# Performance work log

Measured on AMD Instinct MI355X. Metric: run time of the kernel, lower is better.

## Reference

```python
import jax, jax.numpy as jnp
import numpy as np

NOISE_DIM = 64
SEQ_DIM = 64
HIDDEN = 512
BATCH = 1024
N_STEPS = 512
INPUT_SIZE = SEQ_DIM + NOISE_DIM + 1  # 129


def setup_inputs() -> dict:
    key = jax.random.key(0)
    ks = jax.random.split(key, 8)
    s = 0.05
    return {
        "noise": jax.random.normal(ks[0], (BATCH, N_STEPS, NOISE_DIM), dtype=jnp.float32),
        "dts": jax.random.uniform(ks[1], (BATCH, N_STEPS, 1), dtype=jnp.float32),
        "W_ih": jax.random.normal(ks[2], (4 * HIDDEN, INPUT_SIZE), dtype=jnp.float32) * s,
        "W_hh": jax.random.normal(ks[3], (4 * HIDDEN, HIDDEN), dtype=jnp.float32) * s,
        "b_ih": jax.random.normal(ks[4], (4 * HIDDEN,), dtype=jnp.float32) * s,
        "b_hh": jax.random.normal(ks[5], (4 * HIDDEN,), dtype=jnp.float32) * s,
        "W_out": jax.random.normal(ks[6], (SEQ_DIM, HIDDEN), dtype=jnp.float32) * s,
        "b_out": jax.random.normal(ks[7], (SEQ_DIM,), dtype=jnp.float32) * s,
    }


def reference(noise, dts, W_ih, W_hh, b_ih, b_hh, W_out, b_out):
    B = noise.shape[0]
    H = W_hh.shape[1]
    last0 = jnp.zeros((B, SEQ_DIM), dtype=noise.dtype)
    h0 = jnp.zeros((B, H), dtype=noise.dtype)
    c0 = jnp.zeros((B, H), dtype=noise.dtype)
    b = b_ih + b_hh

    def step(carry, inp):
        last, h, c = carry
        n_t, dt_t = inp  # (B, noise_dim), (B, 1)
        x = jnp.concatenate([last, n_t, dt_t], axis=-1)  # (B, input_size)
        gates = x @ W_ih.T + h @ W_hh.T + b  # (B, 4H)
        i_g, f_g, g_g, o_g = jnp.split(gates, 4, axis=-1)
        c_new = jax.nn.sigmoid(f_g) * c + jax.nn.sigmoid(i_g) * jnp.tanh(g_g)
        h_new = jax.nn.sigmoid(o_g) * jnp.tanh(c_new)
        y = h_new @ W_out.T + b_out  # (B, seq_dim)
        return (y, h_new, c_new), y

    noise_t = jnp.swapaxes(noise, 0, 1)  # (n, B, noise_dim)
    dts_t = jnp.swapaxes(dts, 0, 1)  # (n, B, 1)
    (last, h, c), ys = jax.lax.scan(step, (last0, h0, c0), (noise_t, dts_t))
    gen_seq = jnp.swapaxes(ys, 0, 1)  # (B, n, seq_dim)
    return gen_seq, h[None, :, :], c[None, :, :]
```

## Files before the change

kernel.cpp:

```cpp
#include <hip/hip_runtime.h>
#include <stdint.h>


#define NGRP 32
#define KF_X 5
#define KF_H 32
#define KF_TOT 37
#define MAIN_FRAGS (8 * 8 * KF_TOT)
#define Y_FRAGS 64
#define TOT_FRAGS (MAIN_FRAGS + Y_FRAGS)
#define HOFF 33554432ull
#define COFF (HOFF + 524288ull)

typedef __attribute__((ext_vector_type(8))) short short8;
typedef __attribute__((ext_vector_type(4))) float f32x4;
typedef __attribute__((ext_vector_type(16))) float f32x16;
typedef __attribute__((ext_vector_type(4))) unsigned int u32x4;

__device__ __forceinline__ unsigned short f2bf(float x) {
  unsigned int u = __float_as_uint(x);
  u += 0x7FFFu + ((u >> 16) & 1u);
  return (unsigned short)(u >> 16);
}
__device__ __forceinline__ unsigned int pk2(float a, float b) {
  return (unsigned)f2bf(a) | ((unsigned)f2bf(b) << 16);
}
__device__ __forceinline__ int uperm(int kz, int hi, int j) {
  return 64 * (kz >> 2) + 16 * (kz & 3) + 8 * (j >> 2) + 2 * (j & 3) + hi;
}

__global__ void prep_pack(const float* __restrict__ Wih,
                          const float* __restrict__ Whh,
                          const float* __restrict__ bih,
                          const float* __restrict__ bhh,
                          const float* __restrict__ Wout,
                          const float* __restrict__ bout,
                          unsigned short* __restrict__ pack,
                          int* __restrict__ flags) {
  int tid = blockIdx.x * blockDim.x + threadIdx.x;
  if (blockIdx.x == 0) {
    for (int i = threadIdx.x; i < NGRP * 256; i += blockDim.x) flags[i] = 0;
  }
  int fi = tid >> 6, l = tid & 63;
  if (fi >= TOT_FRAGS) return;
  int r = l & 31, hi = l >> 5;
  unsigned short o[8];
  if (fi < MAIN_FRAGS) {
    int jwg = fi / (8 * KF_TOT);
    int rem = fi % (8 * KF_TOT);
    int w = rem / KF_TOT, kf = rem % KF_TOT;
    int g2 = r & 3, s = r >> 3, hb = (r >> 2) & 1;
    int row = g2 * 512 + jwg * 64 + w * 8 + 2 * s + hb;
    for (int j = 0; j < 8; ++j) {
      float v;
      if (kf < KF_X) {
        int kx = kf * 16 + 8 * hi + j;
        if (kx < 64) {
          v = Wih[row * 129 + 64 + kx];
        } else if (kx == 64) {
          v = Wih[row * 129 + 128];
        } else if (kx == 65) {
          float a = bih[row] + bhh[row];
          for (int q = 0; q < 64; ++q) a += Wih[row * 129 + q] * bout[q];
          v = a;
        } else if (kx == 66) {
          float a = 0.f;
          for (int q = 0; q < 64; ++q) a -= Wih[row * 129 + q] * bout[q];
          v = a;
        } else {
          v = 0.f;
        }
      } else {
        int kz = kf - KF_X;
        int U = uperm(kz, hi, j);
        float a = Whh[row * 512 + U];
        for (int q = 0; q < 64; ++q) a += Wih[row * 129 + q] * Wout[q * 512 + U];
        v = a;
      }
      o[j] = f2bf(v);
    }
  } else {
    int fy = fi - MAIN_FRAGS;
    int ry = fy >> 5, kz = fy & 31;
    int row = ry * 32 + r;
    for (int j = 0; j < 8; ++j) {
      int U = uperm(kz, hi, j);
      o[j] = f2bf(Wout[row * 512 + U]);
    }
  }
  unsigned short* dst = pack + (size_t)fi * 512 + l * 8;
  for (int j = 0; j < 8; ++j) dst[j] = o[j];
}

#define AGLD(p) \
  __hip_atomic_load((p), __ATOMIC_RELAXED, __HIP_MEMORY_SCOPE_AGENT)
#define AGST(p, v) \
  __hip_atomic_store((p), (v), __ATOMIC_RELAXED, __HIP_MEMORY_SCOPE_AGENT)

__global__ __launch_bounds__(256)
__attribute__((amdgpu_waves_per_eu(1, 1))) void lstm_main(
    const float* __restrict__ noise, const float* __restrict__ dts,
    const unsigned short* __restrict__ pack, const float* __restrict__ bout,
    unsigned short* __restrict__ hbuf, int* __restrict__ flags,
    float* __restrict__ out) {
  __shared__ __align__(16) unsigned short act[KF_TOT * 512];
  __shared__ __align__(16) float ybuf[4 * 64 * 17];
  const int tid = threadIdx.x;
  const int w = tid >> 6, l = tid & 63;
  const int r = l & 31, hi = l >> 5;
  const int bid = blockIdx.x;
  const int jwg = bid >> 5, grp = bid & 31;
  const int bat = grp * 32 + r;

  for (int i = tid; i < (KF_H * 512) / 2; i += 256)
    ((unsigned int*)(act + KF_X * 512))[i] = 0u;

  short8 wA[KF_TOT], wB[KF_TOT];
  {
    const unsigned short* wl =
        pack + (size_t)((jwg * 8 + 2 * w) * KF_TOT) * 512 + l * 8;
#pragma unroll
    for (int kf = 0; kf < KF_TOT; ++kf) {
      wA[kf] = *(const short8*)(wl + (size_t)kf * 512);
      asm volatile("" : "+a"(wA[kf]));
      wB[kf] = *(const short8*)(wl + (size_t)(KF_TOT + kf) * 512);
      if (kf < 16)
        asm volatile("" : "+a"(wB[kf]));
      else
        asm volatile("" : "+v"(wB[kf]));
    }
  }

  float c0[4] = {0.f, 0.f, 0.f, 0.f}, c1[4] = {0.f, 0.f, 0.f, 0.f};
  float h0[4] = {0.f, 0.f, 0.f, 0.f}, h1[4] = {0.f, 0.f, 0.f, 0.f};
  float4 bo = {0.f, 0.f, 0.f, 0.f};
  if (jwg < 2) bo = *(const float4*)(bout + 32 * jwg + 8 * w + 4 * hi);

  auto cell = [&](const f32x16& a, float* cs, float* hs) {
#pragma unroll
    for (int s = 0; s < 4; ++s) {
      float iv = a[4 * s + 0], fv = a[4 * s + 1];
      float gv = a[4 * s + 2], ov = a[4 * s + 3];
      float ig = 1.f / (1.f + __expf(-iv));
      float fg = 1.f / (1.f + __expf(-fv));
      float e2g = __expf(2.f * gv);
      float gg = 1.f - 2.f / (e2g + 1.f);
      float og = 1.f / (1.f + __expf(-ov));
      float cn = fg * cs[s] + ig * gg;
      float e2c = __expf(2.f * cn);
      float tc = 1.f - 2.f / (e2c + 1.f);
      cs[s] = cn;
      hs[s] = og * tc;
    }
  };

  auto y_partial = [&]() {
    const unsigned short* yl =
        pack + (size_t)(MAIN_FRAGS + jwg * 32 + w * 8) * 512 + l * 8;
    f32x16 ya;
#pragma unroll
    for (int i = 0; i < 16; ++i) ya[i] = 0.f;
    short8 ywr[4];
#pragma unroll
    for (int p = 0; p < 4; ++p) ywr[p] = *(const short8*)(yl + (size_t)p * 512);
#pragma unroll
    for (int q = 0; q < 8; ++q) {
      short8 bv = *(const short8*)&act[(KF_X + w * 8 + q) * 512 + l * 8];
      ya = __builtin_amdgcn_mfma_f32_32x32x16_bf16(ywr[q & 3], bv, ya, 0, 0, 0);
      if (q + 4 < 8)
        ywr[q & 3] = *(const short8*)(yl + (size_t)(q + 4) * 512);
    }
#pragma unroll
    for (int s = 0; s < 4; ++s) {
      f32x4 v = {ya[4 * s], ya[4 * s + 1], ya[4 * s + 2], ya[4 * s + 3]};
      *(f32x4*)&ybuf[(w * 64 + l) * 17 + 4 * s] = v;
    }
  };

  auto y_sum = [&](int tw) {
    f32x4 s0 = *(f32x4*)&ybuf[(0 * 64 + l) * 17 + 4 * w];
    f32x4 s1 = *(f32x4*)&ybuf[(1 * 64 + l) * 17 + 4 * w];
    f32x4 s2 = *(f32x4*)&ybuf[(2 * 64 + l) * 17 + 4 * w];
    f32x4 s3 = *(f32x4*)&ybuf[(3 * 64 + l) * 17 + 4 * w];
    float4 o;
    o.x = s0[0] + s1[0] + s2[0] + s3[0] + bo.x;
    o.y = s0[1] + s1[1] + s2[1] + s3[1] + bo.y;
    o.z = s0[2] + s1[2] + s2[2] + s3[2] + bo.z;
    o.w = s0[3] + s1[3] + s2[3] + s3[3] + bo.w;
    *(float4*)(out + ((size_t)bat * 512 + tw) * 64 + 32 * jwg + 8 * w +
               4 * hi) = o;
  };

  {
    const float* np = noise + (size_t)bat * 512 * 64 + w * 16 + 8 * hi;
    float4 f0 = *(const float4*)np;
    float4 f1 = *(const float4*)(np + 4);
    u32x4 d;
    d[0] = pk2(f0.x, f0.y);
    d[1] = pk2(f0.z, f0.w);
    d[2] = pk2(f1.x, f1.y);
    d[3] = pk2(f1.z, f1.w);
    *(u32x4*)&act[w * 512 + l * 8] = d;
    if (w == 0) {
      u32x4 d4 = {0u, 0u, 0u, 0u};
      if (hi == 0) {
        float dt = dts[(size_t)bat * 512];
        d4[0] = pk2(dt, 1.0f);
        d4[1] = pk2(1.0f, 0.0f);
      }
      *(u32x4*)&act[4 * 512 + l * 8] = d4;
    }
  }
  __syncthreads();

  const int kz_own = 4 * jwg + w;

#pragma unroll 1
  for (int t = 0; t < 512; ++t) {
    float4 nf0, nf1;
    float dtv = 0.f;
    if (t < 511) {
      const float* np =
          noise + ((size_t)bat * 512 + t + 1) * 64 + w * 16 + 8 * hi;
      nf0 = *(const float4*)np;
      nf1 = *(const float4*)(np + 4);
      if (w == 0 && hi == 0) dtv = dts[(size_t)bat * 512 + t + 1];
    }

    f32x16 a0, a1;
#pragma unroll
    for (int i = 0; i < 16; ++i) {
      a0[i] = 0.f;
      a1[i] = 0.f;
    }
#pragma unroll
    for (int kf = 0; kf < KF_TOT; ++kf) {
      short8 bv = *(const short8*)&act[kf * 512 + l * 8];
      a0 = __builtin_amdgcn_mfma_f32_32x32x16_bf16(wA[kf], bv, a0, 0, 0, 0);
      a1 = __builtin_amdgcn_mfma_f32_32x32x16_bf16(wB[kf], bv, a1, 0, 0, 0);
    }

    cell(a0, c0, h0);
    cell(a1, c1, h1);

    unsigned int p0 = pk2(h0[0], h0[1]), p1 = pk2(h0[2], h0[3]);
    unsigned int p2 = pk2(h1[0], h1[1]), p3 = pk2(h1[2], h1[3]);
    {
      unsigned long long* hp = (unsigned long long*)(
          hbuf + ((size_t)(grp * 2 + (t & 1)) * KF_H + kz_own) * 512 + l * 8);
      AGST(hp, (unsigned long long)p0 | ((unsigned long long)p1 << 32));
      AGST(hp + 1, (unsigned long long)p2 | ((unsigned long long)p3 << 32));
    }

    if (jwg < 2 && t > 0) y_partial();

    __syncthreads();

    if (tid == 0) AGST(&flags[grp * 256 + jwg * 32], t + 1);

    if (jwg < 2 && t > 0) y_sum(t - 1);

    if (t < 511) {
      u32x4 d;
      d[0] = pk2(nf0.x, nf0.y);
      d[1] = pk2(nf0.z, nf0.w);
      d[2] = pk2(nf1.x, nf1.y);
      d[3] = pk2(nf1.z, nf1.w);
      *(u32x4*)&act[w * 512 + l * 8] = d;
      if (w == 0) {
        u32x4 d4 = {0u, 0u, 0u, 0u};
        if (hi == 0) d4[0] = pk2(dtv, 1.0f);
        *(u32x4*)&act[4 * 512 + l * 8] = d4;
      }
    }

    if (tid < 8) {
      while (AGLD(&flags[grp * 256 + tid * 32]) < t + 1)
        __builtin_amdgcn_s_sleep(1);
    }
    __syncthreads();

    {
      const unsigned long long* src = (const unsigned long long*)(
          hbuf + (size_t)(grp * 2 + (t & 1)) * KF_H * 512);
      unsigned long long q[16];
#pragma unroll
      for (int k = 0; k < 8; ++k) {
        int idx = (4 * k + w) * 128 + l * 2;
        q[2 * k] = AGLD(src + idx);
        q[2 * k + 1] = AGLD(src + idx + 1);
      }
#pragma unroll
      for (int k = 0; k < 8; ++k) {
        u32x4 d;
        d[0] = (unsigned)q[2 * k];
        d[1] = (unsigned)(q[2 * k] >> 32);
        d[2] = (unsigned)q[2 * k + 1];
        d[3] = (unsigned)(q[2 * k + 1] >> 32);
        *(u32x4*)&act[(KF_X + 4 * k + w) * 512 + l * 8] = d;
      }
    }
    __syncthreads();
  }

  if (jwg < 2) y_partial();
  __syncthreads();
  if (jwg < 2) y_sum(511);
#pragma unroll
  for (int s = 0; s < 4; ++s) {
    int U0 = jwg * 64 + (2 * w + 0) * 8 + 2 * s + hi;
    int U1 = jwg * 64 + (2 * w + 1) * 8 + 2 * s + hi;
    out[HOFF + (size_t)bat * 512 + U0] = h0[s];
    out[COFF + (size_t)bat * 512 + U0] = c0[s];
    out[HOFF + (size_t)bat * 512 + U1] = h1[s];
    out[COFF + (size_t)bat * 512 + U1] = c1[s];
  }
}

extern "C" void kernel_launch(void* const* d_in, const int* in_sizes, int n_in,
                              void* d_out, int out_size, void* d_ws,
                              size_t ws_size, hipStream_t stream) {
  (void)in_sizes;
  (void)n_in;
  (void)out_size;
  (void)ws_size;
  const float* noise = (const float*)d_in[0];
  const float* dts = (const float*)d_in[1];
  const float* Wih = (const float*)d_in[2];
  const float* Whh = (const float*)d_in[3];
  const float* bih = (const float*)d_in[4];
  const float* bhh = (const float*)d_in[5];
  const float* Wout = (const float*)d_in[6];
  const float* bout = (const float*)d_in[7];

  unsigned short* pack = (unsigned short*)d_ws;
  unsigned short* hbuf = pack + (size_t)TOT_FRAGS * 512;
  int* flags = (int*)(hbuf + (size_t)NGRP * 2 * KF_H * 512);

  prep_pack<<<(TOT_FRAGS * 64 + 255) / 256, 256, 0, stream>>>(
      Wih, Whh, bih, bhh, Wout, bout, pack, flags);
  lstm_main<<<256, 256, 0, stream>>>(noise, dts, pack, bout, hbuf, flags,
                                     (float*)d_out);
}
```

Baseline: 2.788 ms.

## Add XCC-local fast path for inter-block hidden-state exchange with fallback

Each block records its XCC id. When all 8 blocks of a batch group share one XCC and the workspace is large enough, they exchange hidden state and step flags through a second buffer using sc0-scoped stores and loads, which should stay in that XCC's L2 instead of going through agent-scope coherence. Every step also keeps writing the agent-scope buffer and flags. If the agent-scope flag shows up before the fast one, a trip flag switches the block back to the slow path. This adds duplicate stores, a full vmcnt wait before each barrier, and fragile assumptions about cache coherence.

```diff
diff --git a/kernel.cpp b/kernel.cpp
--- a/kernel.cpp
+++ b/kernel.cpp
@@ -36,10 +36,13 @@
                           const float* __restrict__ Wout,
                           const float* __restrict__ bout,
                           unsigned short* __restrict__ pack,
-                          int* __restrict__ flags) {
+                          int* __restrict__ flags, int* __restrict__ flags2) {
   int tid = blockIdx.x * blockDim.x + threadIdx.x;
   if (blockIdx.x == 0) {
-    for (int i = threadIdx.x; i < NGRP * 256; i += blockDim.x) flags[i] = 0;
+    for (int i = threadIdx.x; i < NGRP * 256; i += blockDim.x) {
+      flags[i] = 0;
+      flags2[i] = 0;
+    }
   }
   int fi = tid >> 6, l = tid & 63;
   if (fi >= TOT_FRAGS) return;
@@ -101,16 +104,26 @@
 __attribute__((amdgpu_waves_per_eu(1, 1))) void lstm_main(
     const float* __restrict__ noise, const float* __restrict__ dts,
     const unsigned short* __restrict__ pack, const float* __restrict__ bout,
-    unsigned short* __restrict__ hbuf, int* __restrict__ flags,
+    unsigned short* __restrict__ hbuf, unsigned short* __restrict__ hbuf2,
+    int* __restrict__ flags, int* __restrict__ flags2, int fastEnable,
     float* __restrict__ out) {
   __shared__ __align__(16) unsigned short act[KF_TOT * 512];
   __shared__ __align__(16) float ybuf[4 * 64 * 17];
+  __shared__ int xshare[8];
+  __shared__ int tripflag;
   const int tid = threadIdx.x;
   const int w = tid >> 6, l = tid & 63;
   const int r = l & 31, hi = l >> 5;
   const int bid = blockIdx.x;
   const int jwg = bid >> 5, grp = bid & 31;
   const int bat = grp * 32 + r;
+  const int fbase = grp * 256;
+
+  if (tid == 0) {
+    unsigned xcc = __builtin_amdgcn_s_getreg((31u << 11) | 20u) & 0xFFu;
+    AGST(&flags2[fbase + jwg * 32 + 16], (int)xcc + 1);
+    tripflag = 0;
+  }
 
   for (int i = tid; i < (KF_H * 512) / 2; i += 256)
     ((unsigned int*)(act + KF_X * 512))[i] = 0u;
@@ -214,9 +227,13 @@
   __syncthreads();
 
   const int kz_own = 4 * jwg + w;
+  bool fast_ok = false;
+  int verdictNew = 0;
 
 #pragma unroll 1
   for (int t = 0; t < 512; ++t) {
+    const int par = t & 1;
+
     float4 nf0, nf1;
     float dtv = 0.f;
     if (t < 511) {
@@ -247,16 +264,37 @@
     unsigned int p2 = pk2(h1[0], h1[1]), p3 = pk2(h1[2], h1[3]);
     {
       unsigned long long* hp = (unsigned long long*)(
-          hbuf + ((size_t)(grp * 2 + (t & 1)) * KF_H + kz_own) * 512 + l * 8);
+          hbuf2 + ((size_t)(grp * 2 + par) * KF_H + kz_own) * 512 + l * 8);
       AGST(hp, (unsigned long long)p0 | ((unsigned long long)p1 << 32));
       AGST(hp + 1, (unsigned long long)p2 | ((unsigned long long)p3 << 32));
+      if (fast_ok) {
+        u32x4 pay;
+        pay[0] = p0;
+        pay[1] = p1;
+        pay[2] = p2;
+        pay[3] = p3;
+        unsigned long long wa =
+            (unsigned long long)hbuf + (unsigned long long)(grp * 2 + par) * 32768ull +
+            (unsigned long long)kz_own * 1024ull + (unsigned long long)l * 16ull;
+        asm volatile("global_store_dwordx4 %0, %1, off sc0" ::"v"(wa), "v"(pay)
+                     : "memory");
+      }
     }
 
     if (jwg < 2 && t > 0) y_partial();
 
+    asm volatile("s_waitcnt vmcnt(0)" ::: "memory");
     __syncthreads();
 
-    if (tid == 0) AGST(&flags[grp * 256 + jwg * 32], t + 1);
+    if (tid == 0) {
+      AGST(&flags2[fbase + jwg * 32], t + 1);
+      if (fast_ok) {
+        unsigned long long fa = (unsigned long long)&flags[fbase + jwg * 32];
+        unsigned tg = (unsigned)(t + 1);
+        asm volatile("global_store_dword %0, %1, off sc0" ::"v"(fa), "v"(tg)
+                     : "memory");
+      }
+    }
 
     if (jwg < 2 && t > 0) y_sum(t - 1);
 
@@ -274,15 +312,77 @@
       }
     }
 
-    if (tid < 8) {
-      while (AGLD(&flags[grp * 256 + tid * 32]) < t + 1)
-        __builtin_amdgcn_s_sleep(1);
+    if (fast_ok) {
+      if (tid < 8) {
+        unsigned long long fa = (unsigned long long)&flags[fbase + tid * 32];
+        const int* f2p = &flags2[fbase + tid * 32];
+        while (1) {
+          unsigned v;
+          asm volatile(
+              "global_load_dword %0, %1, off sc0\n\ts_waitcnt vmcnt(0)"
+              : "=v"(v)
+              : "v"(fa)
+              : "memory");
+          if ((int)v >= t + 1) break;
+          if (AGLD(f2p) >= t + 1) {
+            tripflag = 1;
+            break;
+          }
+        }
+      }
+    } else {
+      if (tid < 8) {
+        while (AGLD(&flags2[fbase + tid * 32]) < t + 1)
+          __builtin_amdgcn_s_sleep(1);
+        if (t == 0) xshare[tid] = AGLD(&flags2[fbase + tid * 32 + 16]);
+      }
     }
     __syncthreads();
 
-    {
+    const int tripped = tripflag;
+    if (t == 0) {
+      int v0 = xshare[0];
+      int eq = (v0 != 0);
+#pragma unroll
+      for (int i = 1; i < 8; ++i) eq &= (xshare[i] == v0);
+      verdictNew = (fastEnable != 0) && eq;
+    }
+
+    if (fast_ok && !tripped) {
+      unsigned long long rb =
+          (unsigned long long)hbuf + (unsigned long long)(grp * 2 + par) * 32768ull +
+          (unsigned long long)w * 1024ull + (unsigned long long)l * 16ull;
+      u32x4 r0, r1, r2, r3, r4, r5, r6, r7;
+      asm volatile(
+          "global_load_dwordx4 %0, %4, off sc0\n\t"
+          "global_load_dwordx4 %1, %5, off sc0\n\t"
+          "global_load_dwordx4 %2, %6, off sc0\n\t"
+          "global_load_dwordx4 %3, %7, off sc0\n\t"
+          "s_waitcnt vmcnt(0)"
+          : "=&v"(r0), "=&v"(r1), "=&v"(r2), "=&v"(r3)
+          : "v"(rb), "v"(rb + 4096ull), "v"(rb + 8192ull), "v"(rb + 12288ull)
+          : "memory");
+      *(u32x4*)&act[(KF_X + 0 + w) * 512 + l * 8] = r0;
+      *(u32x4*)&act[(KF_X + 4 + w) * 512 + l * 8] = r1;
+      *(u32x4*)&act[(KF_X + 8 + w) * 512 + l * 8] = r2;
+      *(u32x4*)&act[(KF_X + 12 + w) * 512 + l * 8] = r3;
+      asm volatile(
+          "global_load_dwordx4 %0, %4, off sc0\n\t"
+          "global_load_dwordx4 %1, %5, off sc0\n\t"
+          "global_load_dwordx4 %2, %6, off sc0\n\t"
+          "global_load_dwordx4 %3, %7, off sc0\n\t"
+          "s_waitcnt vmcnt(0)"
+          : "=&v"(r4), "=&v"(r5), "=&v"(r6), "=&v"(r7)
+          : "v"(rb + 16384ull), "v"(rb + 20480ull), "v"(rb + 24576ull),
+            "v"(rb + 28672ull)
+          : "memory");
+      *(u32x4*)&act[(KF_X + 16 + w) * 512 + l * 8] = r4;
+      *(u32x4*)&act[(KF_X + 20 + w) * 512 + l * 8] = r5;
+      *(u32x4*)&act[(KF_X + 24 + w) * 512 + l * 8] = r6;
+      *(u32x4*)&act[(KF_X + 28 + w) * 512 + l * 8] = r7;
+    } else {
       const unsigned long long* src = (const unsigned long long*)(
-          hbuf + (size_t)(grp * 2 + (t & 1)) * KF_H * 512);
+          hbuf2 + (size_t)(grp * 2 + par) * KF_H * 512);
       unsigned long long q[16];
 #pragma unroll
       for (int k = 0; k < 8; ++k) {
@@ -300,7 +400,11 @@
         *(u32x4*)&act[(KF_X + 4 * k + w) * 512 + l * 8] = d;
       }
     }
+    if (tid == 0) tripflag = 0;
     __syncthreads();
+
+    if (tripped) fast_ok = false;
+    if (t == 0) fast_ok = (verdictNew != 0);
   }
 
   if (jwg < 2) y_partial();
@@ -323,7 +427,6 @@
   (void)in_sizes;
   (void)n_in;
   (void)out_size;
-  (void)ws_size;
   const float* noise = (const float*)d_in[0];
   const float* dts = (const float*)d_in[1];
   const float* Wih = (const float*)d_in[2];
@@ -335,10 +438,24 @@
 
   unsigned short* pack = (unsigned short*)d_ws;
   unsigned short* hbuf = pack + (size_t)TOT_FRAGS * 512;
-  int* flags = (int*)(hbuf + (size_t)NGRP * 2 * KF_H * 512);
+  unsigned short* hbuf2;
+  int *flags, *flags2;
+  int fastEnable;
+  const size_t need = 2490368ull + 2097152ull * 2 + 65536ull;
+  if (ws_size >= need) {
+    hbuf2 = hbuf + 1048576;
+    flags = (int*)(hbuf2 + 1048576);
+    flags2 = flags + 8192;
+    fastEnable = 1;
+  } else {
+    hbuf2 = hbuf;
+    flags = (int*)(hbuf + 1048576);
+    flags2 = flags;
+    fastEnable = 0;
+  }
 
   prep_pack<<<(TOT_FRAGS * 64 + 255) / 256, 256, 0, stream>>>(
-      Wih, Whh, bih, bhh, Wout, bout, pack, flags);
-  lstm_main<<<256, 256, 0, stream>>>(noise, dts, pack, bout, hbuf, flags,
-                                     (float*)d_out);
-}
+      Wih, Whh, bih, bhh, Wout, bout, pack, flags, flags2);
+  lstm_main<<<256, 256, 0, stream>>>(noise, dts, pack, bout, hbuf, hbuf2,
+                                     flags, flags2, fastEnable, (float*)d_out);
+}
```

Result: no change. 2.841 ms (+1.9%).

## Replace flag polling with step-tagged hidden-state exchange between workgroups

Applied to the files above, without the earlier changes.

Each hidden-state store now interleaves the step number with the packed bf16 values in 16-byte chunks, written with inline-asm system-coherent dwordx4 stores. Consumers load the chunks directly and re-poll only the chunks whose tags do not match yet. This removes the separate flag spin and its extra barrier from the per-step cross-workgroup handoff, and falls back to flag polling after a long spin. The exchange buffer doubles in size and relies on 16-byte stores landing atomically. The old flag-based kernel is kept as a fallback when the workspace is too small.

```diff
diff --git a/kernel.cpp b/kernel.cpp
--- a/kernel.cpp
+++ b/kernel.cpp
@@ -98,10 +98,10 @@
   __hip_atomic_store((p), (v), __ATOMIC_RELAXED, __HIP_MEMORY_SCOPE_AGENT)
 
 __global__ __launch_bounds__(256)
-__attribute__((amdgpu_waves_per_eu(1, 1))) void lstm_main(
+__attribute__((amdgpu_waves_per_eu(1, 1))) void lstm_tag(
     const float* __restrict__ noise, const float* __restrict__ dts,
     const unsigned short* __restrict__ pack, const float* __restrict__ bout,
-    unsigned short* __restrict__ hbuf, int* __restrict__ flags,
+    unsigned int* __restrict__ hbuf, int* __restrict__ flags,
     float* __restrict__ out) {
   __shared__ __align__(16) unsigned short act[KF_TOT * 512];
   __shared__ __align__(16) float ybuf[4 * 64 * 17];
@@ -111,6 +111,9 @@
   const int bid = blockIdx.x;
   const int jwg = bid >> 5, grp = bid & 31;
   const int bat = grp * 32 + r;
+  const int fbase = grp * 256;
+  const unsigned long long hb =
+      (unsigned long long)hbuf + (unsigned long long)grp * 131072ull;
 
   for (int i = tid; i < (KF_H * 512) / 2; i += 256)
     ((unsigned int*)(act + KF_X * 512))[i] = 0u;
@@ -214,9 +217,14 @@
   __syncthreads();
 
   const int kz_own = 4 * jwg + w;
+  const unsigned long long wadr0 =
+      hb + (unsigned long long)kz_own * 2048ull + (unsigned long long)l * 32ull;
 
 #pragma unroll 1
   for (int t = 0; t < 512; ++t) {
+    const int par = t & 1;
+    const unsigned tg = (unsigned)(t + 1);
+
     float4 nf0, nf1;
     float dtv = 0.f;
     if (t < 511) {
@@ -243,20 +251,30 @@
     cell(a0, c0, h0);
     cell(a1, c1, h1);
 
-    unsigned int p0 = pk2(h0[0], h0[1]), p1 = pk2(h0[2], h0[3]);
-    unsigned int p2 = pk2(h1[0], h1[1]), p3 = pk2(h1[2], h1[3]);
     {
-      unsigned long long* hp = (unsigned long long*)(
-          hbuf + ((size_t)(grp * 2 + (t & 1)) * KF_H + kz_own) * 512 + l * 8);
-      AGST(hp, (unsigned long long)p0 | ((unsigned long long)p1 << 32));
-      AGST(hp + 1, (unsigned long long)p2 | ((unsigned long long)p3 << 32));
+      u32x4 s0, s1;
+      s0[0] = tg;
+      s0[1] = pk2(h0[0], h0[1]);
+      s0[2] = tg;
+      s0[3] = pk2(h0[2], h0[3]);
+      s1[0] = tg;
+      s1[1] = pk2(h1[0], h1[1]);
+      s1[2] = tg;
+      s1[3] = pk2(h1[2], h1[3]);
+      unsigned long long wa = wadr0 + (unsigned long long)par * 65536ull;
+      asm volatile(
+          "global_store_dwordx4 %0, %1, off sc0 sc1\n\t"
+          "global_store_dwordx4 %0, %2, off offset:16 sc0 sc1" ::"v"(wa),
+          "v"(s0), "v"(s1)
+          : "memory");
     }
 
     if (jwg < 2 && t > 0) y_partial();
 
+    asm volatile("s_waitcnt vmcnt(0)" ::: "memory");
     __syncthreads();
 
-    if (tid == 0) AGST(&flags[grp * 256 + jwg * 32], t + 1);
+    if (tid == 0) AGST(&flags[fbase + jwg * 32], t + 1);
 
     if (jwg < 2 && t > 0) y_sum(t - 1);
 
@@ -274,6 +292,289 @@
       }
     }
 
+    {
+      const unsigned long long rb = hb + (unsigned long long)par * 65536ull +
+                                    (unsigned long long)l * 32ull;
+      unsigned long long b0 = rb + (unsigned long long)(4 * 0 + w) * 2048ull;
+      unsigned long long b1 = rb + (unsigned long long)(4 * 1 + w) * 2048ull;
+      unsigned long long b2 = rb + (unsigned long long)(4 * 2 + w) * 2048ull;
+      unsigned long long b3 = rb + (unsigned long long)(4 * 3 + w) * 2048ull;
+      unsigned long long b4 = rb + (unsigned long long)(4 * 4 + w) * 2048ull;
+      unsigned long long b5 = rb + (unsigned long long)(4 * 5 + w) * 2048ull;
+      unsigned long long b6 = rb + (unsigned long long)(4 * 6 + w) * 2048ull;
+      unsigned long long b7 = rb + (unsigned long long)(4 * 7 + w) * 2048ull;
+      u32x4 q0, q1, q2, q3, q4, q5, q6, q7;
+      u32x4 q8, q9, q10, q11, q12, q13, q14, q15;
+      asm volatile(
+          "global_load_dwordx4 %0, %16, off sc0 sc1\n\t"
+          "global_load_dwordx4 %1, %16, off offset:16 sc0 sc1\n\t"
+          "global_load_dwordx4 %2, %17, off sc0 sc1\n\t"
+          "global_load_dwordx4 %3, %17, off offset:16 sc0 sc1\n\t"
+          "global_load_dwordx4 %4, %18, off sc0 sc1\n\t"
+          "global_load_dwordx4 %5, %18, off offset:16 sc0 sc1\n\t"
+          "global_load_dwordx4 %6, %19, off sc0 sc1\n\t"
+          "global_load_dwordx4 %7, %19, off offset:16 sc0 sc1\n\t"
+          "global_load_dwordx4 %8, %20, off sc0 sc1\n\t"
+          "global_load_dwordx4 %9, %20, off offset:16 sc0 sc1\n\t"
+          "global_load_dwordx4 %10, %21, off sc0 sc1\n\t"
+          "global_load_dwordx4 %11, %21, off offset:16 sc0 sc1\n\t"
+          "global_load_dwordx4 %12, %22, off sc0 sc1\n\t"
+          "global_load_dwordx4 %13, %22, off offset:16 sc0 sc1\n\t"
+          "global_load_dwordx4 %14, %23, off sc0 sc1\n\t"
+          "global_load_dwordx4 %15, %23, off offset:16 sc0 sc1\n\t"
+          "s_waitcnt vmcnt(0)"
+          : "=&v"(q0), "=&v"(q1), "=&v"(q2), "=&v"(q3), "=&v"(q4), "=&v"(q5),
+            "=&v"(q6), "=&v"(q7), "=&v"(q8), "=&v"(q9), "=&v"(q10),
+            "=&v"(q11), "=&v"(q12), "=&v"(q13), "=&v"(q14), "=&v"(q15)
+          : "v"(b0), "v"(b1), "v"(b2), "v"(b3), "v"(b4), "v"(b5), "v"(b6),
+            "v"(b7)
+          : "memory");
+
+      auto fix = [&](u32x4& q, unsigned long long ad, int owner) {
+        int spin = 0;
+        while (q[0] != tg || q[2] != tg) {
+          ++spin;
+          if (spin == 20000) {
+            const int* fp = &flags[fbase + owner * 32];
+            while (AGLD(fp) < (int)tg) __builtin_amdgcn_s_sleep(8);
+          }
+          asm volatile(
+              "global_load_dwordx4 %0, %1, off sc0 sc1\n\ts_waitcnt vmcnt(0)"
+              : "=v"(q)
+              : "v"(ad)
+              : "memory");
+        }
+      };
+      fix(q0, b0, 0);
+      fix(q1, b0 + 16ull, 0);
+      fix(q2, b1, 1);
+      fix(q3, b1 + 16ull, 1);
+      fix(q4, b2, 2);
+      fix(q5, b2 + 16ull, 2);
+      fix(q6, b3, 3);
+      fix(q7, b3 + 16ull, 3);
+      fix(q8, b4, 4);
+      fix(q9, b4 + 16ull, 4);
+      fix(q10, b5, 5);
+      fix(q11, b5 + 16ull, 5);
+      fix(q12, b6, 6);
+      fix(q13, b6 + 16ull, 6);
+      fix(q14, b7, 7);
+      fix(q15, b7 + 16ull, 7);
+
+#define WRF(k, qa, qb)                                     \
+  {                                                        \
+    u32x4 d;                                               \
+    d[0] = qa[1];                                          \
+    d[1] = qa[3];                                          \
+    d[2] = qb[1];                                          \
+    d[3] = qb[3];                                          \
+    *(u32x4*)&act[(KF_X + 4 * k + w) * 512 + l * 8] = d;   \
+  }
+      WRF(0, q0, q1)
+      WRF(1, q2, q3)
+      WRF(2, q4, q5)
+      WRF(3, q6, q7)
+      WRF(4, q8, q9)
+      WRF(5, q10, q11)
+      WRF(6, q12, q13)
+      WRF(7, q14, q15)
+#undef WRF
+    }
+    __syncthreads();
+  }
+
+  if (jwg < 2) y_partial();
+  __syncthreads();
+  if (jwg < 2) y_sum(511);
+#pragma unroll
+  for (int s = 0; s < 4; ++s) {
+    int U0 = jwg * 64 + (2 * w + 0) * 8 + 2 * s + hi;
+    int U1 = jwg * 64 + (2 * w + 1) * 8 + 2 * s + hi;
+    out[HOFF + (size_t)bat * 512 + U0] = h0[s];
+    out[COFF + (size_t)bat * 512 + U0] = c0[s];
+    out[HOFF + (size_t)bat * 512 + U1] = h1[s];
+    out[COFF + (size_t)bat * 512 + U1] = c1[s];
+  }
+}
+
+__global__ __launch_bounds__(256)
+__attribute__((amdgpu_waves_per_eu(1, 1))) void lstm_flag(
+    const float* __restrict__ noise, const float* __restrict__ dts,
+    const unsigned short* __restrict__ pack, const float* __restrict__ bout,
+    unsigned short* __restrict__ hbuf, int* __restrict__ flags,
+    float* __restrict__ out) {
+  __shared__ __align__(16) unsigned short act[KF_TOT * 512];
+  __shared__ __align__(16) float ybuf[4 * 64 * 17];
+  const int tid = threadIdx.x;
+  const int w = tid >> 6, l = tid & 63;
+  const int r = l & 31, hi = l >> 5;
+  const int bid = blockIdx.x;
+  const int jwg = bid >> 5, grp = bid & 31;
+  const int bat = grp * 32 + r;
+
+  for (int i = tid; i < (KF_H * 512) / 2; i += 256)
+    ((unsigned int*)(act + KF_X * 512))[i] = 0u;
+
+  short8 wA[KF_TOT], wB[KF_TOT];
+  {
+    const unsigned short* wl =
+        pack + (size_t)((jwg * 8 + 2 * w) * KF_TOT) * 512 + l * 8;
+#pragma unroll
+    for (int kf = 0; kf < KF_TOT; ++kf) {
+      wA[kf] = *(const short8*)(wl + (size_t)kf * 512);
+      asm volatile("" : "+a"(wA[kf]));
+      wB[kf] = *(const short8*)(wl + (size_t)(KF_TOT + kf) * 512);
+      if (kf < 16)
+        asm volatile("" : "+a"(wB[kf]));
+      else
+        asm volatile("" : "+v"(wB[kf]));
+    }
+  }
+
+  float c0[4] = {0.f, 0.f, 0.f, 0.f}, c1[4] = {0.f, 0.f, 0.f, 0.f};
+  float h0[4] = {0.f, 0.f, 0.f, 0.f}, h1[4] = {0.f, 0.f, 0.f, 0.f};
+  float4 bo = {0.f, 0.f, 0.f, 0.f};
+  if (jwg < 2) bo = *(const float4*)(bout + 32 * jwg + 8 * w + 4 * hi);
+
+  auto cell = [&](const f32x16& a, float* cs, float* hs) {
+#pragma unroll
+    for (int s = 0; s < 4; ++s) {
+      float iv = a[4 * s + 0], fv = a[4 * s + 1];
+      float gv = a[4 * s + 2], ov = a[4 * s + 3];
+      float ig = 1.f / (1.f + __expf(-iv));
+      float fg = 1.f / (1.f + __expf(-fv));
+      float e2g = __expf(2.f * gv);
+      float gg = 1.f - 2.f / (e2g + 1.f);
+      float og = 1.f / (1.f + __expf(-ov));
+      float cn = fg * cs[s] + ig * gg;
+      float e2c = __expf(2.f * cn);
+      float tc = 1.f - 2.f / (e2c + 1.f);
+      cs[s] = cn;
+      hs[s] = og * tc;
+    }
+  };
+
+  auto y_partial = [&]() {
+    const unsigned short* yl =
+        pack + (size_t)(MAIN_FRAGS + jwg * 32 + w * 8) * 512 + l * 8;
+    f32x16 ya;
+#pragma unroll
+    for (int i = 0; i < 16; ++i) ya[i] = 0.f;
+    short8 ywr[4];
+#pragma unroll
+    for (int p = 0; p < 4; ++p) ywr[p] = *(const short8*)(yl + (size_t)p * 512);
+#pragma unroll
+    for (int q = 0; q < 8; ++q) {
+      short8 bv = *(const short8*)&act[(KF_X + w * 8 + q) * 512 + l * 8];
+      ya = __builtin_amdgcn_mfma_f32_32x32x16_bf16(ywr[q & 3], bv, ya, 0, 0, 0);
+      if (q + 4 < 8)
+        ywr[q & 3] = *(const short8*)(yl + (size_t)(q + 4) * 512);
+    }
+#pragma unroll
+    for (int s = 0; s < 4; ++s) {
+      f32x4 v = {ya[4 * s], ya[4 * s + 1], ya[4 * s + 2], ya[4 * s + 3]};
+      *(f32x4*)&ybuf[(w * 64 + l) * 17 + 4 * s] = v;
+    }
+  };
+
+  auto y_sum = [&](int tw) {
+    f32x4 s0 = *(f32x4*)&ybuf[(0 * 64 + l) * 17 + 4 * w];
+    f32x4 s1 = *(f32x4*)&ybuf[(1 * 64 + l) * 17 + 4 * w];
+    f32x4 s2 = *(f32x4*)&ybuf[(2 * 64 + l) * 17 + 4 * w];
+    f32x4 s3 = *(f32x4*)&ybuf[(3 * 64 + l) * 17 + 4 * w];
+    float4 o;
+    o.x = s0[0] + s1[0] + s2[0] + s3[0] + bo.x;
+    o.y = s0[1] + s1[1] + s2[1] + s3[1] + bo.y;
+    o.z = s0[2] + s1[2] + s2[2] + s3[2] + bo.z;
+    o.w = s0[3] + s1[3] + s2[3] + s3[3] + bo.w;
+    *(float4*)(out + ((size_t)bat * 512 + tw) * 64 + 32 * jwg + 8 * w +
+               4 * hi) = o;
+  };
+
+  {
+    const float* np = noise + (size_t)bat * 512 * 64 + w * 16 + 8 * hi;
+    float4 f0 = *(const float4*)np;
+    float4 f1 = *(const float4*)(np + 4);
+    u32x4 d;
+    d[0] = pk2(f0.x, f0.y);
+    d[1] = pk2(f0.z, f0.w);
+    d[2] = pk2(f1.x, f1.y);
+    d[3] = pk2(f1.z, f1.w);
+    *(u32x4*)&act[w * 512 + l * 8] = d;
+    if (w == 0) {
+      u32x4 d4 = {0u, 0u, 0u, 0u};
+      if (hi == 0) {
+        float dt = dts[(size_t)bat * 512];
+        d4[0] = pk2(dt, 1.0f);
+        d4[1] = pk2(1.0f, 0.0f);
+      }
+      *(u32x4*)&act[4 * 512 + l * 8] = d4;
+    }
+  }
+  __syncthreads();
+
+  const int kz_own = 4 * jwg + w;
+
+#pragma unroll 1
+  for (int t = 0; t < 512; ++t) {
+    float4 nf0, nf1;
+    float dtv = 0.f;
+    if (t < 511) {
+      const float* np =
+          noise + ((size_t)bat * 512 + t + 1) * 64 + w * 16 + 8 * hi;
+      nf0 = *(const float4*)np;
+      nf1 = *(const float4*)(np + 4);
+      if (w == 0 && hi == 0) dtv = dts[(size_t)bat * 512 + t + 1];
+    }
+
+    f32x16 a0, a1;
+#pragma unroll
+    for (int i = 0; i < 16; ++i) {
+      a0[i] = 0.f;
+      a1[i] = 0.f;
+    }
+#pragma unroll
+    for (int kf = 0; kf < KF_TOT; ++kf) {
+      short8 bv = *(const short8*)&act[kf * 512 + l * 8];
+      a0 = __builtin_amdgcn_mfma_f32_32x32x16_bf16(wA[kf], bv, a0, 0, 0, 0);
+      a1 = __builtin_amdgcn_mfma_f32_32x32x16_bf16(wB[kf], bv, a1, 0, 0, 0);
+    }
+
+    cell(a0, c0, h0);
+    cell(a1, c1, h1);
+
+    unsigned int p0 = pk2(h0[0], h0[1]), p1 = pk2(h0[2], h0[3]);
+    unsigned int p2 = pk2(h1[0], h1[1]), p3 = pk2(h1[2], h1[3]);
+    {
+      unsigned long long* hp = (unsigned long long*)(
+          hbuf + ((size_t)(grp * 2 + (t & 1)) * KF_H + kz_own) * 512 + l * 8);
+      AGST(hp, (unsigned long long)p0 | ((unsigned long long)p1 << 32));
+      AGST(hp + 1, (unsigned long long)p2 | ((unsigned long long)p3 << 32));
+    }
+
+    if (jwg < 2 && t > 0) y_partial();
+
+    __syncthreads();
+
+    if (tid == 0) AGST(&flags[grp * 256 + jwg * 32], t + 1);
+
+    if (jwg < 2 && t > 0) y_sum(t - 1);
+
+    if (t < 511) {
+      u32x4 d;
+      d[0] = pk2(nf0.x, nf0.y);
+      d[1] = pk2(nf0.z, nf0.w);
+      d[2] = pk2(nf1.x, nf1.y);
+      d[3] = pk2(nf1.z, nf1.w);
+      *(u32x4*)&act[w * 512 + l * 8] = d;
+      if (w == 0) {
+        u32x4 d4 = {0u, 0u, 0u, 0u};
+        if (hi == 0) d4[0] = pk2(dtv, 1.0f);
+        *(u32x4*)&act[4 * 512 + l * 8] = d4;
+      }
+    }
+
     if (tid < 8) {
       while (AGLD(&flags[grp * 256 + tid * 32]) < t + 1)
         __builtin_amdgcn_s_sleep(1);
@@ -323,7 +624,6 @@
   (void)in_sizes;
   (void)n_in;
   (void)out_size;
-  (void)ws_size;
   const float* noise = (const float*)d_in[0];
   const float* dts = (const float*)d_in[1];
   const float* Wih = (const float*)d_in[2];
@@ -334,11 +634,23 @@
   const float* bout = (const float*)d_in[7];
 
   unsigned short* pack = (unsigned short*)d_ws;
-  unsigned short* hbuf = pack + (size_t)TOT_FRAGS * 512;
-  int* flags = (int*)(hbuf + (size_t)NGRP * 2 * KF_H * 512);
-
-  prep_pack<<<(TOT_FRAGS * 64 + 255) / 256, 256, 0, stream>>>(
-      Wih, Whh, bih, bhh, Wout, bout, pack, flags);
-  lstm_main<<<256, 256, 0, stream>>>(noise, dts, pack, bout, hbuf, flags,
-                                     (float*)d_out);
+  const size_t packB = (size_t)TOT_FRAGS * 512 * 2;
+  const size_t tagB = (size_t)NGRP * 131072;
+  const size_t flagB = (size_t)NGRP * 256 * 4;
+
+  if (ws_size >= packB + tagB + flagB) {
+    unsigned int* hbuf = (unsigned int*)((char*)d_ws + packB);
+    int* flags = (int*)((char*)d_ws + packB + tagB);
+    prep_pack<<<(TOT_FRAGS * 64 + 255) / 256, 256, 0, stream>>>(
+        Wih, Whh, bih, bhh, Wout, bout, pack, flags);
+    lstm_tag<<<256, 256, 0, stream>>>(noise, dts, pack, bout, hbuf, flags,
+                                      (float*)d_out);
+  } else {
+    unsigned short* hbuf = pack + (size_t)TOT_FRAGS * 512;
+    int* flags = (int*)(hbuf + (size_t)NGRP * 2 * KF_H * 512);
+    prep_pack<<<(TOT_FRAGS * 64 + 255) / 256, 256, 0, stream>>>(
+        Wih, Whh, bih, bhh, Wout, bout, pack, flags);
+    lstm_flag<<<256, 256, 0, stream>>>(noise, dts, pack, bout, hbuf, flags,
+                                       (float*)d_out);
+  }
 }
```

Result: slower. 3.569 ms (+28.0%).

## Ping-pong two batch groups per workgroup to hide cross-block sync latency

Applied to the files above, without the earlier changes.

Halves the grid to 128 workgroups, with each workgroup handling two 32-row batch groups in alternation and keeping separate LDS activation buffers and register state for each. While one group waits on the flag exchange for the other workgroups' hidden state, the other group's MFMA and cell work can proceed, which is meant to overlap the inter-workgroup synchronisation latency with compute. In exchange it doubles the per-workgroup work, halves the number of active CUs, and adds extra barriers and register pressure from the duplicated h/c state.

```diff
diff --git a/kernel.cpp b/kernel.cpp
--- a/kernel.cpp
+++ b/kernel.cpp
@@ -16,6 +16,11 @@
 typedef __attribute__((ext_vector_type(4))) float f32x4;
 typedef __attribute__((ext_vector_type(16))) float f32x16;
 typedef __attribute__((ext_vector_type(4))) unsigned int u32x4;
+
+template <int N>
+struct IC {
+  static constexpr int value = N;
+};
 
 __device__ __forceinline__ unsigned short f2bf(float x) {
   unsigned int u = __float_as_uint(x);
@@ -98,22 +103,23 @@
   __hip_atomic_store((p), (v), __ATOMIC_RELAXED, __HIP_MEMORY_SCOPE_AGENT)
 
 __global__ __launch_bounds__(256)
-__attribute__((amdgpu_waves_per_eu(1, 1))) void lstm_main(
+__attribute__((amdgpu_waves_per_eu(1, 1))) void lstm_pp(
     const float* __restrict__ noise, const float* __restrict__ dts,
     const unsigned short* __restrict__ pack, const float* __restrict__ bout,
     unsigned short* __restrict__ hbuf, int* __restrict__ flags,
     float* __restrict__ out) {
-  __shared__ __align__(16) unsigned short act[KF_TOT * 512];
-  __shared__ __align__(16) float ybuf[4 * 64 * 17];
+  __shared__ __align__(16) unsigned short act[2][KF_TOT * 512];
+  __shared__ __align__(16) float ybuf[2][4 * 64 * 17];
   const int tid = threadIdx.x;
   const int w = tid >> 6, l = tid & 63;
   const int r = l & 31, hi = l >> 5;
   const int bid = blockIdx.x;
-  const int jwg = bid >> 5, grp = bid & 31;
-  const int bat = grp * 32 + r;
-
-  for (int i = tid; i < (KF_H * 512) / 2; i += 256)
-    ((unsigned int*)(act + KF_X * 512))[i] = 0u;
+  const int jwg = bid >> 4, grp = bid & 15;
+
+  for (int i = tid; i < (KF_H * 512) / 2; i += 256) {
+    ((unsigned int*)(act[0] + KF_X * 512))[i] = 0u;
+    ((unsigned int*)(act[1] + KF_X * 512))[i] = 0u;
+  }
 
   short8 wA[KF_TOT], wB[KF_TOT];
   {
@@ -131,12 +137,14 @@
     }
   }
 
-  float c0[4] = {0.f, 0.f, 0.f, 0.f}, c1[4] = {0.f, 0.f, 0.f, 0.f};
-  float h0[4] = {0.f, 0.f, 0.f, 0.f}, h1[4] = {0.f, 0.f, 0.f, 0.f};
+  float cst[2][2][4] = {};
+  float hst[2][2][4] = {};
   float4 bo = {0.f, 0.f, 0.f, 0.f};
   if (jwg < 2) bo = *(const float4*)(bout + 32 * jwg + 8 * w + 4 * hi);
 
-  auto cell = [&](const f32x16& a, float* cs, float* hs) {
+  const int kz_own = 4 * jwg + w;
+
+  auto cellf = [&](const f32x16& a, float* cs, float* hs) {
 #pragma unroll
     for (int s = 0; s < 4; ++s) {
       float iv = a[4 * s + 0], fv = a[4 * s + 1];
@@ -154,7 +162,7 @@
     }
   };
 
-  auto y_partial = [&]() {
+  auto y_partial = [&](unsigned short* actc, float* ybc) {
     const unsigned short* yl =
         pack + (size_t)(MAIN_FRAGS + jwg * 32 + w * 8) * 512 + l * 8;
     f32x16 ya;
@@ -165,7 +173,7 @@
     for (int p = 0; p < 4; ++p) ywr[p] = *(const short8*)(yl + (size_t)p * 512);
 #pragma unroll
     for (int q = 0; q < 8; ++q) {
-      short8 bv = *(const short8*)&act[(KF_X + w * 8 + q) * 512 + l * 8];
+      short8 bv = *(const short8*)&actc[(KF_X + w * 8 + q) * 512 + l * 8];
       ya = __builtin_amdgcn_mfma_f32_32x32x16_bf16(ywr[q & 3], bv, ya, 0, 0, 0);
       if (q + 4 < 8)
         ywr[q & 3] = *(const short8*)(yl + (size_t)(q + 4) * 512);
@@ -173,15 +181,15 @@
 #pragma unroll
     for (int s = 0; s < 4; ++s) {
       f32x4 v = {ya[4 * s], ya[4 * s + 1], ya[4 * s + 2], ya[4 * s + 3]};
-      *(f32x4*)&ybuf[(w * 64 + l) * 17 + 4 * s] = v;
-    }
-  };
-
-  auto y_sum = [&](int tw) {
-    f32x4 s0 = *(f32x4*)&ybuf[(0 * 64 + l) * 17 + 4 * w];
-    f32x4 s1 = *(f32x4*)&ybuf[(1 * 64 + l) * 17 + 4 * w];
-    f32x4 s2 = *(f32x4*)&ybuf[(2 * 64 + l) * 17 + 4 * w];
-    f32x4 s3 = *(f32x4*)&ybuf[(3 * 64 + l) * 17 + 4 * w];
+      *(f32x4*)&ybc[(w * 64 + l) * 17 + 4 * s] = v;
+    }
+  };
+
+  auto y_sum = [&](int tw, int bat, float* ybc) {
+    f32x4 s0 = *(f32x4*)&ybc[(0 * 64 + l) * 17 + 4 * w];
+    f32x4 s1 = *(f32x4*)&ybc[(1 * 64 + l) * 17 + 4 * w];
+    f32x4 s2 = *(f32x4*)&ybc[(2 * 64 + l) * 17 + 4 * w];
+    f32x4 s3 = *(f32x4*)&ybc[(3 * 64 + l) * 17 + 4 * w];
     float4 o;
     o.x = s0[0] + s1[0] + s2[0] + s3[0] + bo.x;
     o.y = s0[1] + s1[1] + s2[1] + s3[1] + bo.y;
@@ -191,7 +199,8 @@
                4 * hi) = o;
   };
 
-  {
+  auto stage_x0 = [&](int c) {
+    int bat = (grp * 2 + c) * 32 + r;
     const float* np = noise + (size_t)bat * 512 * 64 + w * 16 + 8 * hi;
     float4 f0 = *(const float4*)np;
     float4 f1 = *(const float4*)(np + 4);
@@ -200,7 +209,7 @@
     d[1] = pk2(f0.z, f0.w);
     d[2] = pk2(f1.x, f1.y);
     d[3] = pk2(f1.z, f1.w);
-    *(u32x4*)&act[w * 512 + l * 8] = d;
+    *(u32x4*)&act[c][w * 512 + l * 8] = d;
     if (w == 0) {
       u32x4 d4 = {0u, 0u, 0u, 0u};
       if (hi == 0) {
@@ -208,15 +217,20 @@
         d4[0] = pk2(dt, 1.0f);
         d4[1] = pk2(1.0f, 0.0f);
       }
-      *(u32x4*)&act[4 * 512 + l * 8] = d4;
-    }
-  }
+      *(u32x4*)&act[c][4 * 512 + l * 8] = d4;
+    }
+  };
+  stage_x0(0);
+  stage_x0(1);
   __syncthreads();
 
-  const int kz_own = 4 * jwg + w;
-
-#pragma unroll 1
-  for (int t = 0; t < 512; ++t) {
+  auto phase = [&](auto CC, int t) {
+    constexpr int c = CC.value;
+    const int gc = grp * 2 + c;
+    const int bat = gc * 32 + r;
+    const int par = t & 1;
+    unsigned short* actc = act[c];
+
     float4 nf0, nf1;
     float dtv = 0.f;
     if (t < 511) {
@@ -235,30 +249,32 @@
     }
 #pragma unroll
     for (int kf = 0; kf < KF_TOT; ++kf) {
-      short8 bv = *(const short8*)&act[kf * 512 + l * 8];
+      short8 bv = *(const short8*)&actc[kf * 512 + l * 8];
       a0 = __builtin_amdgcn_mfma_f32_32x32x16_bf16(wA[kf], bv, a0, 0, 0, 0);
       a1 = __builtin_amdgcn_mfma_f32_32x32x16_bf16(wB[kf], bv, a1, 0, 0, 0);
     }
 
-    cell(a0, c0, h0);
-    cell(a1, c1, h1);
-
-    unsigned int p0 = pk2(h0[0], h0[1]), p1 = pk2(h0[2], h0[3]);
-    unsigned int p2 = pk2(h1[0], h1[1]), p3 = pk2(h1[2], h1[3]);
+    cellf(a0, cst[c][0], hst[c][0]);
+    cellf(a1, cst[c][1], hst[c][1]);
+
     {
+      unsigned int p0 = pk2(hst[c][0][0], hst[c][0][1]);
+      unsigned int p1 = pk2(hst[c][0][2], hst[c][0][3]);
+      unsigned int p2 = pk2(hst[c][1][0], hst[c][1][1]);
+      unsigned int p3 = pk2(hst[c][1][2], hst[c][1][3]);
       unsigned long long* hp = (unsigned long long*)(
-          hbuf + ((size_t)(grp * 2 + (t & 1)) * KF_H + kz_own) * 512 + l * 8);
+          hbuf + ((size_t)(gc * 2 + par) * KF_H + kz_own) * 512 + l * 8);
       AGST(hp, (unsigned long long)p0 | ((unsigned long long)p1 << 32));
       AGST(hp + 1, (unsigned long long)p2 | ((unsigned long long)p3 << 32));
     }
 
-    if (jwg < 2 && t > 0) y_partial();
+    if (jwg < 2 && t > 0) y_partial(actc, ybuf[c]);
 
     __syncthreads();
 
-    if (tid == 0) AGST(&flags[grp * 256 + jwg * 32], t + 1);
-
-    if (jwg < 2 && t > 0) y_sum(t - 1);
+    if (tid == 0) AGST(&flags[gc * 256 + jwg * 32], t + 1);
+
+    if (jwg < 2 && t > 0) y_sum(t - 1, bat, ybuf[c]);
 
     if (t < 511) {
       u32x4 d;
@@ -266,54 +282,81 @@
       d[1] = pk2(nf0.z, nf0.w);
       d[2] = pk2(nf1.x, nf1.y);
       d[3] = pk2(nf1.z, nf1.w);
-      *(u32x4*)&act[w * 512 + l * 8] = d;
+      *(u32x4*)&actc[w * 512 + l * 8] = d;
       if (w == 0) {
         u32x4 d4 = {0u, 0u, 0u, 0u};
         if (hi == 0) d4[0] = pk2(dtv, 1.0f);
-        *(u32x4*)&act[4 * 512 + l * 8] = d4;
+        *(u32x4*)&actc[4 * 512 + l * 8] = d4;
       }
     }
+  };
+
+  auto refill = [&](auto CC, int t) {
+    constexpr int c = CC.value;
+    const int gc = grp * 2 + c;
+    const int par = t & 1;
+    const unsigned long long* src = (const unsigned long long*)(
+        hbuf + (size_t)(gc * 2 + par) * KF_H * 512);
+    unsigned long long q[16];
+#pragma unroll
+    for (int k = 0; k < 8; ++k) {
+      int idx = (4 * k + w) * 128 + l * 2;
+      q[2 * k] = AGLD(src + idx);
+      q[2 * k + 1] = AGLD(src + idx + 1);
+    }
+#pragma unroll
+    for (int k = 0; k < 8; ++k) {
+      u32x4 d;
+      d[0] = (unsigned)q[2 * k];
+      d[1] = (unsigned)(q[2 * k] >> 32);
+      d[2] = (unsigned)q[2 * k + 1];
+      d[3] = (unsigned)(q[2 * k + 1] >> 32);
+      *(u32x4*)&act[c][(KF_X + 4 * k + w) * 512 + l * 8] = d;
+    }
+  };
+
+#pragma unroll 1
+  for (int t = 0; t < 512; ++t) {
+    phase(IC<0>{}, t);
+    phase(IC<1>{}, t);
 
     if (tid < 8) {
-      while (AGLD(&flags[grp * 256 + tid * 32]) < t + 1)
+      while (AGLD(&flags[(grp * 2 + 0) * 256 + tid * 32]) < t + 1)
         __builtin_amdgcn_s_sleep(1);
     }
     __syncthreads();
-
-    {
-      const unsigned long long* src = (const unsigned long long*)(
-          hbuf + (size_t)(grp * 2 + (t & 1)) * KF_H * 512);
-      unsigned long long q[16];
-#pragma unroll
-      for (int k = 0; k < 8; ++k) {
-        int idx = (4 * k + w) * 128 + l * 2;
-        q[2 * k] = AGLD(src + idx);
-        q[2 * k + 1] = AGLD(src + idx + 1);
-      }
-#pragma unroll
-      for (int k = 0; k < 8; ++k) {
-        u32x4 d;
-        d[0] = (unsigned)q[2 * k];
-        d[1] = (unsigned)(q[2 * k] >> 32);
-        d[2] = (unsigned)q[2 * k + 1];
-        d[3] = (unsigned)(q[2 * k + 1] >> 32);
-        *(u32x4*)&act[(KF_X + 4 * k + w) * 512 + l * 8] = d;
-      }
+    refill(IC<0>{}, t);
+
+    if (tid < 8) {
+      while (AGLD(&flags[(grp * 2 + 1) * 256 + tid * 32]) < t + 1)
+        __builtin_amdgcn_s_sleep(1);
     }
     __syncthreads();
-  }
-
-  if (jwg < 2) y_partial();
+    refill(IC<1>{}, t);
+    __syncthreads();
+  }
+
+  if (jwg < 2) {
+    y_partial(act[0], ybuf[0]);
+    y_partial(act[1], ybuf[1]);
+  }
   __syncthreads();
-  if (jwg < 2) y_sum(511);
-#pragma unroll
-  for (int s = 0; s < 4; ++s) {
-    int U0 = jwg * 64 + (2 * w + 0) * 8 + 2 * s + hi;
-    int U1 = jwg * 64 + (2 * w + 1) * 8 + 2 * s + hi;
-    out[HOFF + (size_t)bat * 512 + U0] = h0[s];
-    out[COFF + (size_t)bat * 512 + U0] = c0[s];
-    out[HOFF + (size_t)bat * 512 + U1] = h1[s];
-    out[COFF + (size_t)bat * 512 + U1] = c1[s];
+  if (jwg < 2) {
+    y_sum(511, (grp * 2 + 0) * 32 + r, ybuf[0]);
+    y_sum(511, (grp * 2 + 1) * 32 + r, ybuf[1]);
+  }
+#pragma unroll
+  for (int c = 0; c < 2; ++c) {
+    int bat = (grp * 2 + c) * 32 + r;
+#pragma unroll
+    for (int s = 0; s < 4; ++s) {
+      int U0 = jwg * 64 + (2 * w + 0) * 8 + 2 * s + hi;
+      int U1 = jwg * 64 + (2 * w + 1) * 8 + 2 * s + hi;
+      out[HOFF + (size_t)bat * 512 + U0] = hst[c][0][s];
+      out[COFF + (size_t)bat * 512 + U0] = cst[c][0][s];
+      out[HOFF + (size_t)bat * 512 + U1] = hst[c][1][s];
+      out[COFF + (size_t)bat * 512 + U1] = cst[c][1][s];
+    }
   }
 }
 
@@ -339,6 +382,6 @@
 
   prep_pack<<<(TOT_FRAGS * 64 + 255) / 256, 256, 0, stream>>>(
       Wih, Whh, bih, bhh, Wout, bout, pack, flags);
-  lstm_main<<<256, 256, 0, stream>>>(noise, dts, pack, bout, hbuf, flags,
-                                     (float*)d_out);
-}
+  lstm_pp<<<128, 256, 0, stream>>>(noise, dts, pack, bout, hbuf, flags,
+                                   (float*)d_out);
+}
```

Measured after the change: 5.520 ms. 1.98x slower.
